# Kernel tuning notes

Hardware: AMD Instinct MI355X
Metric: run time of the kernel (lower is better)

## Reference

```python
import jax, jax.numpy as jnp
import numpy as np

B, U, I, H = 1024, 8, 512, 512


def setup_inputs() -> dict:
    key = jax.random.key(0)
    ks = jax.random.split(key, 6)
    s_i = 1.0 / np.sqrt(H)  # torch GRU init: U(-1/sqrt(H), 1/sqrt(H))
    inputs = jax.random.normal(ks[0], (B, U, I), dtype=jnp.float32)
    hidden = jax.random.normal(ks[1], (B, U, H), dtype=jnp.float32)
    W_ih = jax.random.uniform(ks[2], (U, 3 * H, I), minval=-s_i, maxval=s_i, dtype=jnp.float32)
    W_hh = jax.random.uniform(ks[3], (U, 3 * H, H), minval=-s_i, maxval=s_i, dtype=jnp.float32)
    b_ih = jax.random.uniform(ks[4], (U, 3 * H), minval=-s_i, maxval=s_i, dtype=jnp.float32)
    b_hh = jax.random.uniform(ks[5], (U, 3 * H), minval=-s_i, maxval=s_i, dtype=jnp.float32)
    return {"inputs": inputs, "hidden": hidden, "W_ih": W_ih, "W_hh": W_hh, "b_ih": b_ih, "b_hh": b_hh}


def reference(inputs, hidden, W_ih, W_hh, b_ih, b_hh):
    # Grouped single-step GRU: all num_units cells computed in one batched matmul pair.
    # gx, gh: [B, U, 3H]
    gx = jnp.einsum('bui,ugi->bug', inputs, W_ih) + b_ih[None]
    gh = jnp.einsum('buh,ugh->bug', hidden, W_hh) + b_hh[None]
    xr, xz, xn = jnp.split(gx, 3, axis=-1)
    hr, hz, hn = jnp.split(gh, 3, axis=-1)
    r = jax.nn.sigmoid(xr + hr)
    z = jax.nn.sigmoid(xz + hz)
    n = jnp.tanh(xn + r * hn)
    return (1.0 - z) * n + z * hidden
```

## Files before the change

kernel.cpp:

```cpp
#include <hip/hip_runtime.h>
#include <hip/hip_bf16.h>
#include <stdint.h>


#define B_ 1024
#define U_ 8
#define I_ 512
#define H_ 512
#define KDIM 512
#define BM 64
#define BN 64
#define BK 32
#define LSTR 40
#define ESTR 68

typedef __attribute__((ext_vector_type(8))) short short8;
typedef __attribute__((ext_vector_type(4))) float floatx4;

union SmemU {
    short bf[8][BM * LSTR];
    float ep[3][BM * ESTR];
};

__device__ __forceinline__ unsigned int pk2bf(float a, float b) {
    float2 f2; f2.x = a; f2.y = b;
    union { __hip_bfloat162 h; unsigned int u; } cv;
    cv.h = __float22bfloat162_rn(f2);
    return cv.u;
}

__global__ __launch_bounds__(512, 4)
void gru_fused_kernel(const float* __restrict__ inputs,
                      const float* __restrict__ hidden,
                      const float* __restrict__ W_ih,
                      const float* __restrict__ W_hh,
                      const float* __restrict__ b_ih,
                      const float* __restrict__ b_hh,
                      float* __restrict__ out)
{
    const int nb = blockIdx.x;
    const int mb = blockIdx.y;
    const int u  = blockIdx.z;
    const int b0 = mb * BM;
    const int h0 = nb * BN;

    const int tid  = threadIdx.x;
    const int lane = tid & 63;
    const int wave = tid >> 6;
    const int lr   = lane & 15;
    const int q    = lane >> 4;
    const int wm   = wave & 1;
    const int wn   = (wave >> 1) & 1;
    const int g2   = wave >> 2;

    __shared__ SmemU smem;

    const float* srcs[8];
    int rstr[8];
    srcs[0] = inputs + ((size_t)b0 * U_ + u) * I_;           rstr[0] = U_ * I_;
    srcs[1] = hidden + ((size_t)b0 * U_ + u) * H_;           rstr[1] = U_ * H_;
    srcs[2] = W_ih + ((size_t)(u * 3 + 0) * H_ + h0) * I_;   rstr[2] = I_;
    srcs[3] = W_ih + ((size_t)(u * 3 + 1) * H_ + h0) * I_;   rstr[3] = I_;
    srcs[4] = W_ih + ((size_t)(u * 3 + 2) * H_ + h0) * I_;   rstr[4] = I_;
    srcs[5] = W_hh + ((size_t)(u * 3 + 0) * H_ + h0) * H_;   rstr[5] = H_;
    srcs[6] = W_hh + ((size_t)(u * 3 + 1) * H_ + h0) * H_;   rstr[6] = H_;
    srcs[7] = W_hh + ((size_t)(u * 3 + 2) * H_ + h0) * H_;   rstr[7] = H_;

    const int srow = tid >> 3;
    const int c4   = (tid & 7) * 4;
    const float* tb[8];
    #pragma unroll
    for (int s = 0; s < 8; ++s) tb[s] = srcs[s] + (size_t)srow * rstr[s] + c4;

    floatx4 acc[3][2][2];
    #pragma unroll
    for (int g = 0; g < 3; ++g)
        #pragma unroll
        for (int mt = 0; mt < 2; ++mt)
            #pragma unroll
            for (int nt = 0; nt < 2; ++nt)
                acc[g][mt][nt] = (floatx4){0.f, 0.f, 0.f, 0.f};

    const int aslab = g2;
    const int bbase = 2 + 3 * g2;

    float4 pre[8];
    #pragma unroll
    for (int s = 0; s < 8; ++s) pre[s] = *(const float4*)(tb[s]);

    for (int k0 = 0; k0 < KDIM; k0 += BK) {
        #pragma unroll
        for (int s = 0; s < 8; ++s) {
            uint2 w;
            w.x = pk2bf(pre[s].x, pre[s].y);
            w.y = pk2bf(pre[s].z, pre[s].w);
            *(uint2*)&smem.bf[s][srow * LSTR + c4] = w;
        }
        __syncthreads();

        if (k0 + BK < KDIM) {
            #pragma unroll
            for (int s = 0; s < 8; ++s) pre[s] = *(const float4*)(tb[s] + k0 + BK);
        }

        short8 afr[2];
        #pragma unroll
        for (int mt = 0; mt < 2; ++mt)
            afr[mt] = *(const short8*)&smem.bf[aslab][(wm * 32 + mt * 16 + lr) * LSTR + q * 8];
        #pragma unroll
        for (int g = 0; g < 3; ++g) {
            const short8 bf0 = *(const short8*)&smem.bf[bbase + g][(wn * 32 + lr) * LSTR + q * 8];
            const short8 bf1 = *(const short8*)&smem.bf[bbase + g][(wn * 32 + 16 + lr) * LSTR + q * 8];
            #pragma unroll
            for (int mt = 0; mt < 2; ++mt) {
                acc[g][mt][0] = __builtin_amdgcn_mfma_f32_16x16x32_bf16(afr[mt], bf0, acc[g][mt][0], 0, 0, 0);
                acc[g][mt][1] = __builtin_amdgcn_mfma_f32_16x16x32_bf16(afr[mt], bf1, acc[g][mt][1], 0, 0, 0);
            }
        }
        __syncthreads();
    }

    const float* bih = b_ih + u * (3 * H_);
    const float* bhh = b_hh + u * (3 * H_);

    if (g2 == 1) {
        #pragma unroll
        for (int nt = 0; nt < 2; ++nt) {
            const int col = wn * 32 + nt * 16 + lr;
            const float bhr = bhh[h0 + col];
            const float bhz = bhh[H_ + h0 + col];
            const float bhn = bhh[2 * H_ + h0 + col];
            #pragma unroll
            for (int mt = 0; mt < 2; ++mt) {
                #pragma unroll
                for (int r = 0; r < 4; ++r) {
                    const int row = wm * 32 + mt * 16 + q * 4 + r;
                    smem.ep[0][row * ESTR + col] = acc[0][mt][nt][r] + bhr;
                    smem.ep[1][row * ESTR + col] = acc[1][mt][nt][r] + bhz;
                    smem.ep[2][row * ESTR + col] = acc[2][mt][nt][r] + bhn;
                }
            }
        }
    }
    __syncthreads();

    if (g2 == 0) {
        #pragma unroll
        for (int nt = 0; nt < 2; ++nt) {
            const int col  = wn * 32 + nt * 16 + lr;
            const int hcol = h0 + col;
            const float bir  = bih[hcol];
            const float biz  = bih[H_ + hcol];
            const float bin_ = bih[2 * H_ + hcol];
            #pragma unroll
            for (int mt = 0; mt < 2; ++mt) {
                #pragma unroll
                for (int r = 0; r < 4; ++r) {
                    const int row  = wm * 32 + mt * 16 + q * 4 + r;
                    const int brow = b0 + row;
                    const size_t gidx = ((size_t)brow * U_ + u) * H_ + hcol;
                    const float hprev = hidden[gidx];
                    const float hr = smem.ep[0][row * ESTR + col];
                    const float hz = smem.ep[1][row * ESTR + col];
                    const float hn = smem.ep[2][row * ESTR + col];
                    const float xr = acc[0][mt][nt][r] + bir;
                    const float xz = acc[1][mt][nt][r] + biz;
                    const float xn = acc[2][mt][nt][r] + bin_;
                    const float rg = 1.f / (1.f + __expf(-(xr + hr)));
                    const float zg = 1.f / (1.f + __expf(-(xz + hz)));
                    const float ng = tanhf(xn + rg * hn);
                    out[gidx] = (1.f - zg) * ng + zg * hprev;
                }
            }
        }
    }
}

extern "C" void kernel_launch(void* const* d_in, const int* in_sizes, int n_in,
                              void* d_out, int out_size, void* d_ws, size_t ws_size,
                              hipStream_t stream) {
    const float* inputs = (const float*)d_in[0];
    const float* hidden = (const float*)d_in[1];
    const float* W_ih   = (const float*)d_in[2];
    const float* W_hh   = (const float*)d_in[3];
    const float* b_ih   = (const float*)d_in[4];
    const float* b_hh   = (const float*)d_in[5];
    float* out = (float*)d_out;

    dim3 grid(H_ / BN, B_ / BM, U_);
    dim3 block(512);
    gru_fused_kernel<<<grid, block, 0, stream>>>(inputs, hidden, W_ih, W_hh,
                                                 b_ih, b_hh, out);
}
```

Baseline: 194.9 us.

## Pre-convert operands to bf16 in workspace and load tiles via async global-to-LDS

Adds a pre-pass kernel that converts inputs, hidden and both weight tensors to bf16 in the workspace. The main GEMM kernel then streams bf16 tiles directly into LDS with global_load_lds, using an XOR-swizzled layout, BK=64 and a grid reordered so unit and column blocks sit together. This removes the per-tile fp32 register loads and conversions and halves the bytes moved per tile. The cost is an extra full pass that reads fp32 and writes bf16 for all operands, and the loop no longer prefetches the next tile into registers before computing. A fallback path keeps the old kernel for when the workspace is too small.

```diff
diff --git a/kernel.cpp b/kernel.cpp
--- a/kernel.cpp
+++ b/kernel.cpp
@@ -8,19 +8,23 @@
 #define I_ 512
 #define H_ 512
 #define KDIM 512
+
+#define NX (B_ * U_ * I_)
+#define NW (U_ * 3 * H_ * I_)
+#define OFF_X 0
+#define OFF_H NX
+#define OFF_WIH (2 * NX)
+#define OFF_WHH (2 * NX + NW)
+#define NTOT (2 * NX + 2 * NW)
+#define WS_NEED ((size_t)NTOT * 2)
+
 #define BM 64
 #define BN 64
-#define BK 32
-#define LSTR 40
+#define BK 64
 #define ESTR 68
 
 typedef __attribute__((ext_vector_type(8))) short short8;
 typedef __attribute__((ext_vector_type(4))) float floatx4;
-
-union SmemU {
-    short bf[8][BM * LSTR];
-    float ep[3][BM * ESTR];
-};
 
 __device__ __forceinline__ unsigned int pk2bf(float a, float b) {
     float2 f2; f2.x = a; f2.y = b;
@@ -29,18 +33,48 @@
     return cv.u;
 }
 
+__device__ __forceinline__ void async16(const void* g, void* l) {
+    __builtin_amdgcn_global_load_lds(
+        (const __attribute__((address_space(1))) void*)g,
+        (__attribute__((address_space(3))) void*)l, 16, 0, 0);
+}
+
+__global__ __launch_bounds__(256)
+void convert_bf16_kernel(const float* __restrict__ x, const float* __restrict__ h,
+                         const float* __restrict__ wih, const float* __restrict__ whh,
+                         unsigned short* __restrict__ ws)
+{
+    const size_t base = ((size_t)blockIdx.x * 256 + threadIdx.x) * 8;
+    const float* src; size_t off;
+    if (base < (size_t)OFF_H)        { src = x;   off = OFF_X; }
+    else if (base < (size_t)OFF_WIH) { src = h;   off = OFF_H; }
+    else if (base < (size_t)OFF_WHH) { src = wih; off = OFF_WIH; }
+    else                             { src = whh; off = OFF_WHH; }
+    const float4 v0 = *(const float4*)(src + (base - off));
+    const float4 v1 = *(const float4*)(src + (base - off) + 4);
+    uint4 o;
+    o.x = pk2bf(v0.x, v0.y);
+    o.y = pk2bf(v0.z, v0.w);
+    o.z = pk2bf(v1.x, v1.y);
+    o.w = pk2bf(v1.z, v1.w);
+    *(uint4*)(ws + base) = o;
+}
+
+union Smem {
+    unsigned short bf[8][64 * 64];
+    float ep[3][BM * ESTR];
+};
+
 __global__ __launch_bounds__(512, 4)
-void gru_fused_kernel(const float* __restrict__ inputs,
-                      const float* __restrict__ hidden,
-                      const float* __restrict__ W_ih,
-                      const float* __restrict__ W_hh,
-                      const float* __restrict__ b_ih,
-                      const float* __restrict__ b_hh,
-                      float* __restrict__ out)
+void gru_main_kernel(const unsigned short* __restrict__ ws,
+                     const float* __restrict__ hidden,
+                     const float* __restrict__ b_ih,
+                     const float* __restrict__ b_hh,
+                     float* __restrict__ out)
 {
-    const int nb = blockIdx.x;
+    const int u  = blockIdx.x >> 3;
+    const int nb = blockIdx.x & 7;
     const int mb = blockIdx.y;
-    const int u  = blockIdx.z;
     const int b0 = mb * BM;
     const int h0 = nb * BN;
 
@@ -53,24 +87,16 @@
     const int wn   = (wave >> 1) & 1;
     const int g2   = wave >> 2;
 
-    __shared__ SmemU smem;
-
-    const float* srcs[8];
-    int rstr[8];
-    srcs[0] = inputs + ((size_t)b0 * U_ + u) * I_;           rstr[0] = U_ * I_;
-    srcs[1] = hidden + ((size_t)b0 * U_ + u) * H_;           rstr[1] = U_ * H_;
-    srcs[2] = W_ih + ((size_t)(u * 3 + 0) * H_ + h0) * I_;   rstr[2] = I_;
-    srcs[3] = W_ih + ((size_t)(u * 3 + 1) * H_ + h0) * I_;   rstr[3] = I_;
-    srcs[4] = W_ih + ((size_t)(u * 3 + 2) * H_ + h0) * I_;   rstr[4] = I_;
-    srcs[5] = W_hh + ((size_t)(u * 3 + 0) * H_ + h0) * H_;   rstr[5] = H_;
-    srcs[6] = W_hh + ((size_t)(u * 3 + 1) * H_ + h0) * H_;   rstr[6] = H_;
-    srcs[7] = W_hh + ((size_t)(u * 3 + 2) * H_ + h0) * H_;   rstr[7] = H_;
-
-    const int srow = tid >> 3;
-    const int c4   = (tid & 7) * 4;
-    const float* tb[8];
-    #pragma unroll
-    for (int s = 0; s < 8; ++s) tb[s] = srcs[s] + (size_t)srow * rstr[s] + c4;
+    __shared__ Smem smem;
+
+    const unsigned short* gbase; int grstr;
+    if (wave == 0)      { gbase = ws + OFF_X + ((size_t)b0 * U_ + u) * I_; grstr = U_ * I_; }
+    else if (wave == 1) { gbase = ws + OFF_H + ((size_t)b0 * U_ + u) * H_; grstr = U_ * H_; }
+    else if (wave <= 4) { int g = wave - 2; gbase = ws + OFF_WIH + ((size_t)(u * 3 + g) * H_ + h0) * I_; grstr = I_; }
+    else                { int g = wave - 5; gbase = ws + OFF_WHH + ((size_t)(u * 3 + g) * H_ + h0) * H_; grstr = H_; }
+
+    const int rsub = lane >> 3;
+    const int lch  = (lane & 7) ^ rsub;
 
     floatx4 acc[3][2][2];
     #pragma unroll
@@ -84,39 +110,39 @@
     const int aslab = g2;
     const int bbase = 2 + 3 * g2;
 
-    float4 pre[8];
-    #pragma unroll
-    for (int s = 0; s < 8; ++s) pre[s] = *(const float4*)(tb[s]);
-
     for (int k0 = 0; k0 < KDIM; k0 += BK) {
         #pragma unroll
-        for (int s = 0; s < 8; ++s) {
-            uint2 w;
-            w.x = pk2bf(pre[s].x, pre[s].y);
-            w.y = pk2bf(pre[s].z, pre[s].w);
-            *(uint2*)&smem.bf[s][srow * LSTR + c4] = w;
+        for (int i = 0; i < 8; ++i) {
+            const int row = i * 8 + rsub;
+            const unsigned short* g = gbase + (size_t)row * grstr + k0 + lch * 8;
+            void* l = (void*)((char*)&smem.bf[wave][i * 512] + lane * 16);
+            async16(g, l);
         }
         __syncthreads();
 
-        if (k0 + BK < KDIM) {
-            #pragma unroll
-            for (int s = 0; s < 8; ++s) pre[s] = *(const float4*)(tb[s] + k0 + BK);
-        }
-
-        short8 afr[2];
+        short8 afr[2][2];
         #pragma unroll
         for (int mt = 0; mt < 2; ++mt)
-            afr[mt] = *(const short8*)&smem.bf[aslab][(wm * 32 + mt * 16 + lr) * LSTR + q * 8];
-        #pragma unroll
-        for (int g = 0; g < 3; ++g) {
-            const short8 bf0 = *(const short8*)&smem.bf[bbase + g][(wn * 32 + lr) * LSTR + q * 8];
-            const short8 bf1 = *(const short8*)&smem.bf[bbase + g][(wn * 32 + 16 + lr) * LSTR + q * 8];
-            #pragma unroll
-            for (int mt = 0; mt < 2; ++mt) {
-                acc[g][mt][0] = __builtin_amdgcn_mfma_f32_16x16x32_bf16(afr[mt], bf0, acc[g][mt][0], 0, 0, 0);
-                acc[g][mt][1] = __builtin_amdgcn_mfma_f32_16x16x32_bf16(afr[mt], bf1, acc[g][mt][1], 0, 0, 0);
+            #pragma unroll
+            for (int ks = 0; ks < 2; ++ks) {
+                const int row = wm * 32 + mt * 16 + lr;
+                const int ch  = (ks * 4 + q) ^ (lr & 7);
+                afr[mt][ks] = *(const short8*)&smem.bf[aslab][row * 64 + ch * 8];
             }
-        }
+        #pragma unroll
+        for (int g = 0; g < 3; ++g)
+            #pragma unroll
+            for (int nt = 0; nt < 2; ++nt)
+                #pragma unroll
+                for (int ks = 0; ks < 2; ++ks) {
+                    const int row = wn * 32 + nt * 16 + lr;
+                    const int ch  = (ks * 4 + q) ^ (lr & 7);
+                    const short8 bfr = *(const short8*)&smem.bf[bbase + g][row * 64 + ch * 8];
+                    #pragma unroll
+                    for (int mt = 0; mt < 2; ++mt)
+                        acc[g][mt][nt] = __builtin_amdgcn_mfma_f32_16x16x32_bf16(
+                            afr[mt][ks], bfr, acc[g][mt][nt], 0, 0, 0);
+                }
         __syncthreads();
     }
 
@@ -131,7 +157,7 @@
             const float bhz = bhh[H_ + h0 + col];
             const float bhn = bhh[2 * H_ + h0 + col];
             #pragma unroll
-            for (int mt = 0; mt < 2; ++mt) {
+            for (int mt = 0; mt < 2; ++mt)
                 #pragma unroll
                 for (int r = 0; r < 4; ++r) {
                     const int row = wm * 32 + mt * 16 + q * 4 + r;
@@ -139,7 +165,6 @@
                     smem.ep[1][row * ESTR + col] = acc[1][mt][nt][r] + bhz;
                     smem.ep[2][row * ESTR + col] = acc[2][mt][nt][r] + bhn;
                 }
-            }
         }
     }
     __syncthreads();
@@ -153,12 +178,11 @@
             const float biz  = bih[H_ + hcol];
             const float bin_ = bih[2 * H_ + hcol];
             #pragma unroll
-            for (int mt = 0; mt < 2; ++mt) {
+            for (int mt = 0; mt < 2; ++mt)
                 #pragma unroll
                 for (int r = 0; r < 4; ++r) {
                     const int row  = wm * 32 + mt * 16 + q * 4 + r;
-                    const int brow = b0 + row;
-                    const size_t gidx = ((size_t)brow * U_ + u) * H_ + hcol;
+                    const size_t gidx = ((size_t)(b0 + row) * U_ + u) * H_ + hcol;
                     const float hprev = hidden[gidx];
                     const float hr = smem.ep[0][row * ESTR + col];
                     const float hz = smem.ep[1][row * ESTR + col];
@@ -171,7 +195,130 @@
                     const float ng = tanhf(xn + rg * hn);
                     out[gidx] = (1.f - zg) * ng + zg * hprev;
                 }
+        }
+    }
+}
+
+#define LSTR 40
+union SmemF {
+    short bf[8][BM * LSTR];
+    float ep[3][BM * ESTR];
+};
+
+__global__ __launch_bounds__(512, 4)
+void gru_fallback_kernel(const float* __restrict__ inputs, const float* __restrict__ hidden,
+                         const float* __restrict__ W_ih, const float* __restrict__ W_hh,
+                         const float* __restrict__ b_ih, const float* __restrict__ b_hh,
+                         float* __restrict__ out)
+{
+    const int nb = blockIdx.x;
+    const int mb = blockIdx.y;
+    const int u  = blockIdx.z;
+    const int b0 = mb * BM, h0 = nb * BN;
+    const int tid = threadIdx.x, lane = tid & 63, wave = tid >> 6;
+    const int lr = lane & 15, q = lane >> 4;
+    const int wm = wave & 1, wn = (wave >> 1) & 1, g2 = wave >> 2;
+
+    __shared__ SmemF smem;
+
+    const float* srcs[8]; int rstr[8];
+    srcs[0] = inputs + ((size_t)b0 * U_ + u) * I_;         rstr[0] = U_ * I_;
+    srcs[1] = hidden + ((size_t)b0 * U_ + u) * H_;         rstr[1] = U_ * H_;
+    srcs[2] = W_ih + ((size_t)(u * 3 + 0) * H_ + h0) * I_; rstr[2] = I_;
+    srcs[3] = W_ih + ((size_t)(u * 3 + 1) * H_ + h0) * I_; rstr[3] = I_;
+    srcs[4] = W_ih + ((size_t)(u * 3 + 2) * H_ + h0) * I_; rstr[4] = I_;
+    srcs[5] = W_hh + ((size_t)(u * 3 + 0) * H_ + h0) * H_; rstr[5] = H_;
+    srcs[6] = W_hh + ((size_t)(u * 3 + 1) * H_ + h0) * H_; rstr[6] = H_;
+    srcs[7] = W_hh + ((size_t)(u * 3 + 2) * H_ + h0) * H_; rstr[7] = H_;
+
+    const int srow = tid >> 3, c4 = (tid & 7) * 4;
+    const float* tb[8];
+    #pragma unroll
+    for (int s = 0; s < 8; ++s) tb[s] = srcs[s] + (size_t)srow * rstr[s] + c4;
+
+    floatx4 acc[3][2][2];
+    #pragma unroll
+    for (int g = 0; g < 3; ++g)
+        #pragma unroll
+        for (int mt = 0; mt < 2; ++mt)
+            #pragma unroll
+            for (int nt = 0; nt < 2; ++nt) acc[g][mt][nt] = (floatx4){0.f, 0.f, 0.f, 0.f};
+
+    const int aslab = g2, bbase = 2 + 3 * g2;
+    float4 pre[8];
+    #pragma unroll
+    for (int s = 0; s < 8; ++s) pre[s] = *(const float4*)(tb[s]);
+
+    for (int k0 = 0; k0 < KDIM; k0 += 32) {
+        #pragma unroll
+        for (int s = 0; s < 8; ++s) {
+            uint2 w; w.x = pk2bf(pre[s].x, pre[s].y); w.y = pk2bf(pre[s].z, pre[s].w);
+            *(uint2*)&smem.bf[s][srow * LSTR + c4] = w;
+        }
+        __syncthreads();
+        if (k0 + 32 < KDIM) {
+            #pragma unroll
+            for (int s = 0; s < 8; ++s) pre[s] = *(const float4*)(tb[s] + k0 + 32);
+        }
+        short8 afr[2];
+        #pragma unroll
+        for (int mt = 0; mt < 2; ++mt)
+            afr[mt] = *(const short8*)&smem.bf[aslab][(wm * 32 + mt * 16 + lr) * LSTR + q * 8];
+        #pragma unroll
+        for (int g = 0; g < 3; ++g) {
+            const short8 bf0 = *(const short8*)&smem.bf[bbase + g][(wn * 32 + lr) * LSTR + q * 8];
+            const short8 bf1 = *(const short8*)&smem.bf[bbase + g][(wn * 32 + 16 + lr) * LSTR + q * 8];
+            #pragma unroll
+            for (int mt = 0; mt < 2; ++mt) {
+                acc[g][mt][0] = __builtin_amdgcn_mfma_f32_16x16x32_bf16(afr[mt], bf0, acc[g][mt][0], 0, 0, 0);
+                acc[g][mt][1] = __builtin_amdgcn_mfma_f32_16x16x32_bf16(afr[mt], bf1, acc[g][mt][1], 0, 0, 0);
             }
+        }
+        __syncthreads();
+    }
+
+    const float* bih = b_ih + u * (3 * H_);
+    const float* bhh = b_hh + u * (3 * H_);
+    if (g2 == 1) {
+        #pragma unroll
+        for (int nt = 0; nt < 2; ++nt) {
+            const int col = wn * 32 + nt * 16 + lr;
+            const float bhr = bhh[h0 + col], bhz = bhh[H_ + h0 + col], bhn = bhh[2 * H_ + h0 + col];
+            #pragma unroll
+            for (int mt = 0; mt < 2; ++mt)
+                #pragma unroll
+                for (int r = 0; r < 4; ++r) {
+                    const int row = wm * 32 + mt * 16 + q * 4 + r;
+                    smem.ep[0][row * ESTR + col] = acc[0][mt][nt][r] + bhr;
+                    smem.ep[1][row * ESTR + col] = acc[1][mt][nt][r] + bhz;
+                    smem.ep[2][row * ESTR + col] = acc[2][mt][nt][r] + bhn;
+                }
+        }
+    }
+    __syncthreads();
+    if (g2 == 0) {
+        #pragma unroll
+        for (int nt = 0; nt < 2; ++nt) {
+            const int col = wn * 32 + nt * 16 + lr, hcol = h0 + col;
+            const float bir = bih[hcol], biz = bih[H_ + hcol], bin_ = bih[2 * H_ + hcol];
+            #pragma unroll
+            for (int mt = 0; mt < 2; ++mt)
+                #pragma unroll
+                for (int r = 0; r < 4; ++r) {
+                    const int row = wm * 32 + mt * 16 + q * 4 + r;
+                    const size_t gidx = ((size_t)(b0 + row) * U_ + u) * H_ + hcol;
+                    const float hprev = hidden[gidx];
+                    const float hr = smem.ep[0][row * ESTR + col];
+                    const float hz = smem.ep[1][row * ESTR + col];
+                    const float hn = smem.ep[2][row * ESTR + col];
+                    const float xr = acc[0][mt][nt][r] + bir;
+                    const float xz = acc[1][mt][nt][r] + biz;
+                    const float xn = acc[2][mt][nt][r] + bin_;
+                    const float rg = 1.f / (1.f + __expf(-(xr + hr)));
+                    const float zg = 1.f / (1.f + __expf(-(xz + hz)));
+                    const float ng = tanhf(xn + rg * hn);
+                    out[gidx] = (1.f - zg) * ng + zg * hprev;
+                }
         }
     }
 }
@@ -187,8 +334,13 @@
     const float* b_hh   = (const float*)d_in[5];
     float* out = (float*)d_out;
 
-    dim3 grid(H_ / BN, B_ / BM, U_);
-    dim3 block(512);
-    gru_fused_kernel<<<grid, block, 0, stream>>>(inputs, hidden, W_ih, W_hh,
-                                                 b_ih, b_hh, out);
-}
+    if (ws_size >= WS_NEED) {
+        unsigned short* ws = (unsigned short*)d_ws;
+        convert_bf16_kernel<<<NTOT / 2048, 256, 0, stream>>>(inputs, hidden, W_ih, W_hh, ws);
+        dim3 grid(64, 16, 1);
+        gru_main_kernel<<<grid, 512, 0, stream>>>(ws, hidden, b_ih, b_hh, out);
+    } else {
+        dim3 grid(8, 16, 8);
+        gru_fallback_kernel<<<grid, 512, 0, stream>>>(inputs, hidden, W_ih, W_hh, b_ih, b_hh, out);
+    }
+}
```

Measured after the change: 201.1 us. 1.03x slower.
